# Kernel tuning notes

Hardware: AMD Instinct MI355X
Metric: run time of the kernel (lower is better)

The kernel has to match this reference:

```python
import jax, jax.numpy as jnp
import numpy as np

B, F, E = 1024, 1024, 256      # batch, flat_shape (mobilenet), embedding_size
L1, L2, L3 = 16, 8, 32         # level1 classes, level2 classes per branch, level3 classes per leaf
NE3 = L1 * L2                  # 128 leaf (level-3) classifier heads


def setup_inputs() -> dict:
    key = jax.random.key(0)
    ks = jax.random.split(key, 10)
    w = lambda k, shape: (jax.random.normal(k, shape, jnp.float32) * 0.02)
    return {
        "features_x": jax.random.normal(ks[0], (B, F), jnp.float32),
        "features_y": jax.random.normal(ks[1], (B, F), jnp.float32),
        # level-1 head: Linear(F->E, no bias) + LayerNorm + ReLU + Linear(E->L1)
        "l1_W1": w(ks[2], (F, E)),
        "l1_g": jnp.ones((E,), jnp.float32), "l1_b": jnp.zeros((E,), jnp.float32),
        "l1_W2": w(ks[3], (E, L1)), "l1_b2": jnp.zeros((L1,), jnp.float32),
        # level-2 heads (one per level-1 class), stacked on a leading expert axis
        "l2_W1": w(ks[4], (L1, F, E)),
        "l2_g": jnp.ones((L1, E), jnp.float32), "l2_b": jnp.zeros((L1, E), jnp.float32),
        "l2_W2": w(ks[5], (L1, E, L2)), "l2_b2": jnp.zeros((L1, L2), jnp.float32),
        # level-3 heads (flattened [level1][level2] -> NE3 experts)
        "l3_W1": w(ks[6], (NE3, F, E)),
        "l3_g": jnp.ones((NE3, E), jnp.float32), "l3_b": jnp.zeros((NE3, E), jnp.float32),
        "l3_W2": w(ks[7], (NE3, E, L3)), "l3_b2": jnp.zeros((NE3, L3), jnp.float32),
    }


def _ln(h, g, b, eps=1e-5):
    m = jnp.mean(h, axis=-1, keepdims=True)
    v = jnp.mean(jnp.square(h - m), axis=-1, keepdims=True)
    return (h - m) * jax.lax.rsqrt(v + eps) * g + b


def reference(features_x, features_y,
              l1_W1, l1_g, l1_b, l1_W2, l1_b2,
              l2_W1, l2_g, l2_b, l2_W2, l2_b2,
              l3_W1, l3_g, l3_b, l3_W2, l3_b2):
    # Dropout is identity in eval mode.
    x, y = features_x, features_y
    rows = jnp.arange(x.shape[0])

    # level 1: single head on x
    h1 = jax.nn.relu(_ln(x @ l1_W1, l1_g, l1_b))
    logits1 = h1 @ l1_W2 + l1_b2                                # [B, L1]
    idx1 = jnp.argmax(logits1, axis=-1)                         # argmax(softmax) == argmax

    # level 2: routed head on 0.6*x + 0.4*y; compute all L1 heads batched, gather selected
    ft = 0.6 * x + 0.4 * y
    h2 = jax.nn.relu(_ln(jnp.einsum('bf,efh->beh', ft, l2_W1), l2_g, l2_b))  # [B, L1, E]
    logits2_all = jnp.einsum('beh,ehc->bec', h2, l2_W2) + l2_b2              # [B, L1, L2]
    logits2 = logits2_all[rows, idx1]                                        # [B, L2]
    idx2 = jnp.argmax(logits2, axis=-1)

    # level 3: doubly-routed head on x; flat expert index = idx1*L2 + idx2
    eidx = idx1 * logits2.shape[-1] + idx2
    h3 = jax.nn.relu(_ln(jnp.einsum('bf,efh->beh', x, l3_W1), l3_g, l3_b))   # [B, NE3, E]
    logits3_all = jnp.einsum('beh,ehc->bec', h3, l3_W2) + l3_b2              # [B, NE3, L3]
    logits3 = logits3_all[rows, eidx]                                        # [B, L3]

    # uniform class counts => pad_sequence is a no-op
    return (logits1, logits2, logits3)
```

## Files before the change

### kernel.cpp

```cpp
#include <hip/hip_runtime.h>

#define B_   1024
#define F_   1024
#define E_   256
#define NL1  16
#define NL2  8
#define NL3  32

__device__ __forceinline__ float b2f(unsigned short u) {
    union { unsigned int i; float f; } v;
    v.i = ((unsigned int)u) << 16;
    return v.f;
}

__device__ __forceinline__ unsigned short f2b(float f) {
    union { float f; unsigned int i; } v;
    v.f = f;
    unsigned int x = v.i;
    x += 0x7fffu + ((x >> 16) & 1u);
    return (unsigned short)(x >> 16);
}

template<int NC>
__device__ void head_row(
    const float* __restrict__ in,
    const void* W1, const void* g, const void* b,
    const void* W2, const void* b2v, int bf,
    float* part,
    float* hn,
    float* red,
    float* lg,
    int t)
{
    const int lane = t & 63;
    const int grp  = t >> 6;
    const int e0   = lane * 4;

    float a0 = 0.f, a1 = 0.f, a2 = 0.f, a3 = 0.f;
    if (bf) {
        const unsigned short* W = (const unsigned short*)W1 + (size_t)grp * 256 * E_;
        for (int ii = 0; ii < 256; ii += 16) {
            ushort4 w[16];
            float   xv[16];
            #pragma unroll
            for (int k = 0; k < 16; ++k) {
                w[k]  = *(const ushort4*)(W + (size_t)(ii + k) * E_ + e0);
                xv[k] = in[grp * 256 + ii + k];
            }
            #pragma unroll
            for (int k = 0; k < 16; ++k) {
                a0 += xv[k] * b2f(w[k].x);
                a1 += xv[k] * b2f(w[k].y);
                a2 += xv[k] * b2f(w[k].z);
                a3 += xv[k] * b2f(w[k].w);
            }
        }
    } else {
        const float* W = (const float*)W1 + (size_t)grp * 256 * E_;
        for (int ii = 0; ii < 256; ii += 8) {
            float4 w[8];
            float  xv[8];
            #pragma unroll
            for (int k = 0; k < 8; ++k) {
                w[k]  = *(const float4*)(W + (size_t)(ii + k) * E_ + e0);
                xv[k] = in[grp * 256 + ii + k];
            }
            #pragma unroll
            for (int k = 0; k < 8; ++k) {
                a0 += xv[k] * w[k].x; a1 += xv[k] * w[k].y;
                a2 += xv[k] * w[k].z; a3 += xv[k] * w[k].w;
            }
        }
    }
    part[grp * E_ + e0 + 0] = a0;
    part[grp * E_ + e0 + 1] = a1;
    part[grp * E_ + e0 + 2] = a2;
    part[grp * E_ + e0 + 3] = a3;
    __syncthreads();

    float h = part[0 * E_ + t] + part[1 * E_ + t] + part[2 * E_ + t] + part[3 * E_ + t];

    float s = h, ss = h * h;
    #pragma unroll
    for (int o = 32; o > 0; o >>= 1) {
        s  += __shfl_xor(s, o);
        ss += __shfl_xor(ss, o);
    }
    if (lane == 0) { red[grp * 2 + 0] = s; red[grp * 2 + 1] = ss; }
    __syncthreads();
    float S  = red[0] + red[2] + red[4] + red[6];
    float SS = red[1] + red[3] + red[5] + red[7];
    float m    = S * (1.0f / E_);
    float var  = SS * (1.0f / E_) - m * m;
    float rstd = rsqrtf(var + 1e-5f);

    float gv, bv;
    if (bf) {
        gv = b2f(((const unsigned short*)g)[t]);
        bv = b2f(((const unsigned short*)b)[t]);
    } else {
        gv = ((const float*)g)[t];
        bv = ((const float*)b)[t];
    }
    hn[t] = fmaxf((h - m) * rstd * gv + bv, 0.0f);
    __syncthreads();

    constexpr int G  = 256 / NC;
    constexpr int CH = E_ / G;
    const int c = t % NC;
    const int j = t / NC;
    float a = 0.f;
    if (bf) {
        const unsigned short* W = (const unsigned short*)W2;
        #pragma unroll 8
        for (int e = j * CH; e < j * CH + CH; ++e) a += hn[e] * b2f(W[(size_t)e * NC + c]);
    } else {
        const float* W = (const float*)W2;
        #pragma unroll 8
        for (int e = j * CH; e < j * CH + CH; ++e) a += hn[e] * W[(size_t)e * NC + c];
    }
    part[j * NC + c] = a;
    __syncthreads();
    #pragma unroll
    for (int sr = G / 2; sr > 0; sr >>= 1) {
        if (j < sr) part[j * NC + c] += part[(j + sr) * NC + c];
        __syncthreads();
    }
    if (t < NC) {
        float bias = bf ? b2f(((const unsigned short*)b2v)[t]) : ((const float*)b2v)[t];
        lg[t] = part[t] + bias;
    }
    __syncthreads();
}

__global__ void dtype_sniff_kernel(const unsigned int* l1g_words, int* flag) {
    if (threadIdx.x == 0 && blockIdx.x == 0) {
        *flag = (l1g_words[0] == 0x3F803F80u) ? 1 : 0;
    }
}

__global__ __launch_bounds__(256, 4) void MultiLevelClassifier_26491358282059_kernel(
    const void* x, const void* y,
    const void* l1W1, const void* l1g, const void* l1b,
    const void* l1W2, const void* l1b2,
    const void* l2W1, const void* l2g, const void* l2b,
    const void* l2W2, const void* l2b2,
    const void* l3W1, const void* l3g, const void* l3b,
    const void* l3W2, const void* l3b2,
    void* out, const int* flagp)
{
    __shared__ float xs[F_];
    __shared__ float fs[F_];
    __shared__ float part[4 * E_];
    __shared__ float hn[E_];
    __shared__ float red[8];
    __shared__ float lg[NL3];
    __shared__ int   sel;

    const int t   = threadIdx.x;
    const int row = blockIdx.x;
    const int bf  = *flagp;

    if (bf) {
        ushort4 xv = ((const ushort4*)x)[(size_t)row * 256 + t];
        ushort4 yv = ((const ushort4*)y)[(size_t)row * 256 + t];
        float x0 = b2f(xv.x), x1 = b2f(xv.y), x2 = b2f(xv.z), x3 = b2f(xv.w);
        xs[t * 4 + 0] = x0; xs[t * 4 + 1] = x1; xs[t * 4 + 2] = x2; xs[t * 4 + 3] = x3;
        fs[t * 4 + 0] = 0.6f * x0 + 0.4f * b2f(yv.x);
        fs[t * 4 + 1] = 0.6f * x1 + 0.4f * b2f(yv.y);
        fs[t * 4 + 2] = 0.6f * x2 + 0.4f * b2f(yv.z);
        fs[t * 4 + 3] = 0.6f * x3 + 0.4f * b2f(yv.w);
    } else {
        float4 xv = ((const float4*)x)[(size_t)row * 256 + t];
        float4 yv = ((const float4*)y)[(size_t)row * 256 + t];
        xs[t * 4 + 0] = xv.x; xs[t * 4 + 1] = xv.y; xs[t * 4 + 2] = xv.z; xs[t * 4 + 3] = xv.w;
        fs[t * 4 + 0] = 0.6f * xv.x + 0.4f * yv.x;
        fs[t * 4 + 1] = 0.6f * xv.y + 0.4f * yv.y;
        fs[t * 4 + 2] = 0.6f * xv.z + 0.4f * yv.z;
        fs[t * 4 + 3] = 0.6f * xv.w + 0.4f * yv.w;
    }
    __syncthreads();

    head_row<NL1>(xs, l1W1, l1g, l1b, l1W2, l1b2, bf, part, hn, red, lg, t);
    if (t < NL1) {
        size_t o = (size_t)row * NL1 + t;
        if (bf) ((unsigned short*)out)[o] = f2b(lg[t]);
        else    ((float*)out)[o] = lg[t];
    }
    if (t == 0) {
        float best = lg[0]; int bi = 0;
        for (int c = 1; c < NL1; ++c)
            if (lg[c] > best) { best = lg[c]; bi = c; }
        sel = bi;
    }
    __syncthreads();
    const int i1 = sel;

    {
        const void* W1 = bf ? (const void*)((const unsigned short*)l2W1 + (size_t)i1 * F_ * E_)
                            : (const void*)((const float*)l2W1 + (size_t)i1 * F_ * E_);
        const void* g  = bf ? (const void*)((const unsigned short*)l2g + (size_t)i1 * E_)
                            : (const void*)((const float*)l2g + (size_t)i1 * E_);
        const void* b  = bf ? (const void*)((const unsigned short*)l2b + (size_t)i1 * E_)
                            : (const void*)((const float*)l2b + (size_t)i1 * E_);
        const void* W2 = bf ? (const void*)((const unsigned short*)l2W2 + (size_t)i1 * E_ * NL2)
                            : (const void*)((const float*)l2W2 + (size_t)i1 * E_ * NL2);
        const void* b2 = bf ? (const void*)((const unsigned short*)l2b2 + (size_t)i1 * NL2)
                            : (const void*)((const float*)l2b2 + (size_t)i1 * NL2);
        head_row<NL2>(fs, W1, g, b, W2, b2, bf, part, hn, red, lg, t);
    }
    if (t < NL2) {
        size_t o = (size_t)B_ * NL1 + (size_t)row * NL2 + t;
        if (bf) ((unsigned short*)out)[o] = f2b(lg[t]);
        else    ((float*)out)[o] = lg[t];
    }
    if (t == 0) {
        float best = lg[0]; int bi = 0;
        for (int c = 1; c < NL2; ++c)
            if (lg[c] > best) { best = lg[c]; bi = c; }
        sel = i1 * NL2 + bi;
    }
    __syncthreads();
    const int e3 = sel;

    {
        const void* W1 = bf ? (const void*)((const unsigned short*)l3W1 + (size_t)e3 * F_ * E_)
                            : (const void*)((const float*)l3W1 + (size_t)e3 * F_ * E_);
        const void* g  = bf ? (const void*)((const unsigned short*)l3g + (size_t)e3 * E_)
                            : (const void*)((const float*)l3g + (size_t)e3 * E_);
        const void* b  = bf ? (const void*)((const unsigned short*)l3b + (size_t)e3 * E_)
                            : (const void*)((const float*)l3b + (size_t)e3 * E_);
        const void* W2 = bf ? (const void*)((const unsigned short*)l3W2 + (size_t)e3 * E_ * NL3)
                            : (const void*)((const float*)l3W2 + (size_t)e3 * E_ * NL3);
        const void* b2 = bf ? (const void*)((const unsigned short*)l3b2 + (size_t)e3 * NL3)
                            : (const void*)((const float*)l3b2 + (size_t)e3 * NL3);
        head_row<NL3>(xs, W1, g, b, W2, b2, bf, part, hn, red, lg, t);
    }
    if (t < NL3) {
        size_t o = (size_t)B_ * (NL1 + NL2) + (size_t)row * NL3 + t;
        if (bf) ((unsigned short*)out)[o] = f2b(lg[t]);
        else    ((float*)out)[o] = lg[t];
    }
}

extern "C" void kernel_launch(void* const* d_in, const int* in_sizes, int n_in,
                              void* d_out, int out_size, void* d_ws, size_t ws_size,
                              hipStream_t stream) {
    (void)in_sizes; (void)n_in; (void)out_size; (void)ws_size;

    int* flag = (int*)d_ws;

    dtype_sniff_kernel<<<1, 1, 0, stream>>>((const unsigned int*)d_in[3], flag);

    MultiLevelClassifier_26491358282059_kernel<<<B_, 256, 0, stream>>>(
        d_in[0], d_in[1],
        d_in[2], d_in[3], d_in[4], d_in[5], d_in[6],
        d_in[7], d_in[8], d_in[9], d_in[10], d_in[11],
        d_in[12], d_in[13], d_in[14], d_in[15], d_in[16],
        d_out, flag);
}
```

Measured before the change: 407.1 us.

## Group rows by routed expert into chunks to reuse expert weights across rows

```diff
diff --git a/kernel.cpp b/kernel.cpp
--- a/kernel.cpp
+++ b/kernel.cpp
@@ -1,31 +1,33 @@
 #include <hip/hip_runtime.h>
 
-#define B_   1024
-#define F_   1024
-#define E_   256
-#define NL1  16
-#define NL2  8
-#define NL3  32
+#define B_    1024
+#define F_    1024
+#define E_    256
+#define NL1   16
+#define NL2   8
+#define NL3   32
+#define NE3_  128
+#define CS1   4
+#define CS    8
+#define MAXCH2 160
+#define MAXCH3 256
+#define OUT2_OFF (B_ * NL1)
+#define OUT3_OFF (B_ * (NL1 + NL2))
 
 __device__ __forceinline__ float b2f(unsigned short u) {
-    union { unsigned int i; float f; } v;
-    v.i = ((unsigned int)u) << 16;
-    return v.f;
-}
-
+    union { unsigned int i; float f; } v; v.i = ((unsigned int)u) << 16; return v.f;
+}
 __device__ __forceinline__ unsigned short f2b(float f) {
-    union { float f; unsigned int i; } v;
-    v.f = f;
-    unsigned int x = v.i;
-    x += 0x7fffu + ((x >> 16) & 1u);
+    union { float f; unsigned int i; } v; v.f = f;
+    unsigned int x = v.i; x += 0x7fffu + ((x >> 16) & 1u);
     return (unsigned short)(x >> 16);
 }
 
-template<int NC>
-__device__ void head_row(
+template<int R, int NC>
+__device__ void head_chunk(
     const float* __restrict__ in,
-    const void* W1, const void* g, const void* b,
-    const void* W2, const void* b2v, int bf,
+    const void* W1v, const void* gv_, const void* bv_,
+    const void* W2v, const void* b2v, int bf,
     float* part,
     float* hn,
     float* red,
@@ -36,210 +38,358 @@
     const int grp  = t >> 6;
     const int e0   = lane * 4;
 
-    float a0 = 0.f, a1 = 0.f, a2 = 0.f, a3 = 0.f;
+    float acc[R][4];
+    #pragma unroll
+    for (int r = 0; r < R; ++r) { acc[r][0]=0.f; acc[r][1]=0.f; acc[r][2]=0.f; acc[r][3]=0.f; }
+
+    const float* ing = in + grp * 256;
+
     if (bf) {
-        const unsigned short* W = (const unsigned short*)W1 + (size_t)grp * 256 * E_;
-        for (int ii = 0; ii < 256; ii += 16) {
+        const unsigned short* W = (const unsigned short*)W1v + (size_t)grp * 256 * E_;
+        for (int f0 = 0; f0 < 256; f0 += 16) {
             ushort4 w[16];
-            float   xv[16];
-            #pragma unroll
-            for (int k = 0; k < 16; ++k) {
-                w[k]  = *(const ushort4*)(W + (size_t)(ii + k) * E_ + e0);
-                xv[k] = in[grp * 256 + ii + k];
+            #pragma unroll
+            for (int k = 0; k < 16; ++k)
+                w[k] = *(const ushort4*)(W + (size_t)(f0 + k) * E_ + e0);
+            #pragma unroll
+            for (int q = 0; q < 4; ++q) {
+                float4 xq[R];
+                #pragma unroll
+                for (int r = 0; r < R; ++r)
+                    xq[r] = *(const float4*)(ing + r * F_ + f0 + q * 4);
+                #pragma unroll
+                for (int k2 = 0; k2 < 4; ++k2) {
+                    ushort4 ww = w[q * 4 + k2];
+                    float w0 = b2f(ww.x), w1 = b2f(ww.y), w2 = b2f(ww.z), w3 = b2f(ww.w);
+                    #pragma unroll
+                    for (int r = 0; r < R; ++r) {
+                        float xv = (k2 == 0) ? xq[r].x : (k2 == 1) ? xq[r].y
+                                 : (k2 == 2) ? xq[r].z : xq[r].w;
+                        acc[r][0] += xv * w0; acc[r][1] += xv * w1;
+                        acc[r][2] += xv * w2; acc[r][3] += xv * w3;
+                    }
+                }
             }
-            #pragma unroll
-            for (int k = 0; k < 16; ++k) {
-                a0 += xv[k] * b2f(w[k].x);
-                a1 += xv[k] * b2f(w[k].y);
-                a2 += xv[k] * b2f(w[k].z);
-                a3 += xv[k] * b2f(w[k].w);
+        }
+    } else {
+        const float* W = (const float*)W1v + (size_t)grp * 256 * E_;
+        for (int f0 = 0; f0 < 256; f0 += 8) {
+            float4 w[8];
+            #pragma unroll
+            for (int k = 0; k < 8; ++k)
+                w[k] = *(const float4*)(W + (size_t)(f0 + k) * E_ + e0);
+            #pragma unroll
+            for (int q = 0; q < 2; ++q) {
+                float4 xq[R];
+                #pragma unroll
+                for (int r = 0; r < R; ++r)
+                    xq[r] = *(const float4*)(ing + r * F_ + f0 + q * 4);
+                #pragma unroll
+                for (int k2 = 0; k2 < 4; ++k2) {
+                    float4 ww = w[q * 4 + k2];
+                    #pragma unroll
+                    for (int r = 0; r < R; ++r) {
+                        float xv = (k2 == 0) ? xq[r].x : (k2 == 1) ? xq[r].y
+                                 : (k2 == 2) ? xq[r].z : xq[r].w;
+                        acc[r][0] += xv * ww.x; acc[r][1] += xv * ww.y;
+                        acc[r][2] += xv * ww.z; acc[r][3] += xv * ww.w;
+                    }
+                }
             }
         }
-    } else {
-        const float* W = (const float*)W1 + (size_t)grp * 256 * E_;
-        for (int ii = 0; ii < 256; ii += 8) {
-            float4 w[8];
-            float  xv[8];
-            #pragma unroll
-            for (int k = 0; k < 8; ++k) {
-                w[k]  = *(const float4*)(W + (size_t)(ii + k) * E_ + e0);
-                xv[k] = in[grp * 256 + ii + k];
-            }
-            #pragma unroll
-            for (int k = 0; k < 8; ++k) {
-                a0 += xv[k] * w[k].x; a1 += xv[k] * w[k].y;
-                a2 += xv[k] * w[k].z; a3 += xv[k] * w[k].w;
-            }
-        }
-    }
-    part[grp * E_ + e0 + 0] = a0;
-    part[grp * E_ + e0 + 1] = a1;
-    part[grp * E_ + e0 + 2] = a2;
-    part[grp * E_ + e0 + 3] = a3;
-    __syncthreads();
-
-    float h = part[0 * E_ + t] + part[1 * E_ + t] + part[2 * E_ + t] + part[3 * E_ + t];
-
-    float s = h, ss = h * h;
-    #pragma unroll
-    for (int o = 32; o > 0; o >>= 1) {
-        s  += __shfl_xor(s, o);
-        ss += __shfl_xor(ss, o);
-    }
-    if (lane == 0) { red[grp * 2 + 0] = s; red[grp * 2 + 1] = ss; }
-    __syncthreads();
-    float S  = red[0] + red[2] + red[4] + red[6];
-    float SS = red[1] + red[3] + red[5] + red[7];
-    float m    = S * (1.0f / E_);
-    float var  = SS * (1.0f / E_) - m * m;
-    float rstd = rsqrtf(var + 1e-5f);
+    }
+
+    #pragma unroll
+    for (int r = 0; r < R; ++r) {
+        part[(size_t)(grp * R + r) * E_ + e0 + 0] = acc[r][0];
+        part[(size_t)(grp * R + r) * E_ + e0 + 1] = acc[r][1];
+        part[(size_t)(grp * R + r) * E_ + e0 + 2] = acc[r][2];
+        part[(size_t)(grp * R + r) * E_ + e0 + 3] = acc[r][3];
+    }
+    __syncthreads();
+
+    float h[R];
+    #pragma unroll
+    for (int r = 0; r < R; ++r)
+        h[r] = part[(0 * R + r) * E_ + t] + part[(1 * R + r) * E_ + t]
+             + part[(2 * R + r) * E_ + t] + part[(3 * R + r) * E_ + t];
+
+    #pragma unroll
+    for (int r = 0; r < R; ++r) {
+        float s = h[r], ss = h[r] * h[r];
+        #pragma unroll
+        for (int o = 32; o > 0; o >>= 1) { s += __shfl_xor(s, o); ss += __shfl_xor(ss, o); }
+        if (lane == 0) { red[(grp * R + r) * 2 + 0] = s; red[(grp * R + r) * 2 + 1] = ss; }
+    }
+    __syncthreads();
 
     float gv, bv;
-    if (bf) {
-        gv = b2f(((const unsigned short*)g)[t]);
-        bv = b2f(((const unsigned short*)b)[t]);
-    } else {
-        gv = ((const float*)g)[t];
-        bv = ((const float*)b)[t];
-    }
-    hn[t] = fmaxf((h - m) * rstd * gv + bv, 0.0f);
-    __syncthreads();
-
-    constexpr int G  = 256 / NC;
+    if (bf) { gv = b2f(((const unsigned short*)gv_)[t]); bv = b2f(((const unsigned short*)bv_)[t]); }
+    else    { gv = ((const float*)gv_)[t];               bv = ((const float*)bv_)[t]; }
+
+    #pragma unroll
+    for (int r = 0; r < R; ++r) {
+        float S  = red[(0*R+r)*2] + red[(1*R+r)*2] + red[(2*R+r)*2] + red[(3*R+r)*2];
+        float SS = red[(0*R+r)*2+1] + red[(1*R+r)*2+1] + red[(2*R+r)*2+1] + red[(3*R+r)*2+1];
+        float m    = S * (1.0f / E_);
+        float var  = SS * (1.0f / E_) - m * m;
+        float rstd = rsqrtf(var + 1e-5f);
+        hn[r * E_ + t] = fmaxf((h[r] - m) * rstd * gv + bv, 0.0f);
+    }
+    __syncthreads();
+
+    constexpr int RN = R * NC;
+    constexpr int G  = 256 / RN;
     constexpr int CH = E_ / G;
-    const int c = t % NC;
-    const int j = t / NC;
+    const int oi = t % RN, j = t / RN, r = oi / NC, c = oi % NC;
     float a = 0.f;
     if (bf) {
-        const unsigned short* W = (const unsigned short*)W2;
+        const unsigned short* W = (const unsigned short*)W2v;
         #pragma unroll 8
-        for (int e = j * CH; e < j * CH + CH; ++e) a += hn[e] * b2f(W[(size_t)e * NC + c]);
+        for (int e = j * CH; e < j * CH + CH; ++e) a += hn[r * E_ + e] * b2f(W[(size_t)e * NC + c]);
     } else {
-        const float* W = (const float*)W2;
+        const float* W = (const float*)W2v;
         #pragma unroll 8
-        for (int e = j * CH; e < j * CH + CH; ++e) a += hn[e] * W[(size_t)e * NC + c];
-    }
-    part[j * NC + c] = a;
-    __syncthreads();
-    #pragma unroll
-    for (int sr = G / 2; sr > 0; sr >>= 1) {
-        if (j < sr) part[j * NC + c] += part[(j + sr) * NC + c];
+        for (int e = j * CH; e < j * CH + CH; ++e) a += hn[r * E_ + e] * W[(size_t)e * NC + c];
+    }
+    float bias = bf ? b2f(((const unsigned short*)b2v)[c]) : ((const float*)b2v)[c];
+    if (G > 1) {
+        part[t] = a;
         __syncthreads();
-    }
-    if (t < NC) {
-        float bias = bf ? b2f(((const unsigned short*)b2v)[t]) : ((const float*)b2v)[t];
-        lg[t] = part[t] + bias;
+        if (j == 0) {
+            float sum = a;
+            #pragma unroll
+            for (int jj = 1; jj < G; ++jj) sum += part[jj * RN + oi];
+            lg[oi] = sum + bias;
+        }
+    } else {
+        lg[oi] = a + bias;
     }
     __syncthreads();
 }
 
 __global__ void dtype_sniff_kernel(const unsigned int* l1g_words, int* flag) {
-    if (threadIdx.x == 0 && blockIdx.x == 0) {
+    if (threadIdx.x == 0 && blockIdx.x == 0)
         *flag = (l1g_words[0] == 0x3F803F80u) ? 1 : 0;
-    }
-}
-
-__global__ __launch_bounds__(256, 4) void MultiLevelClassifier_26491358282059_kernel(
+}
+
+__global__ __launch_bounds__(256) void mlc_level1_kernel(
+    const void* x, const void* W1, const void* g, const void* b,
+    const void* W2, const void* b2, void* out, int* idx1, const int* flagp)
+{
+    __shared__ float in_s[CS1 * F_];
+    __shared__ float part[4 * CS1 * E_];
+    __shared__ float hn[CS1 * E_];
+    __shared__ float red[4 * CS1 * 2];
+    __shared__ float lg[CS1 * NL1];
+
+    const int t = threadIdx.x;
+    const int bf = *flagp;
+    const int row0 = blockIdx.x * CS1;
+
+    #pragma unroll
+    for (int r = 0; r < CS1; ++r) {
+        if (bf) {
+            ushort4 xv = ((const ushort4*)x)[(size_t)(row0 + r) * 256 + t];
+            in_s[r * F_ + t*4+0] = b2f(xv.x); in_s[r * F_ + t*4+1] = b2f(xv.y);
+            in_s[r * F_ + t*4+2] = b2f(xv.z); in_s[r * F_ + t*4+3] = b2f(xv.w);
+        } else {
+            float4 xv = ((const float4*)x)[(size_t)(row0 + r) * 256 + t];
+            in_s[r * F_ + t*4+0] = xv.x; in_s[r * F_ + t*4+1] = xv.y;
+            in_s[r * F_ + t*4+2] = xv.z; in_s[r * F_ + t*4+3] = xv.w;
+        }
+    }
+    __syncthreads();
+
+    head_chunk<CS1, NL1>(in_s, W1, g, b, W2, b2, bf, part, hn, red, lg, t);
+
+    if (t < CS1 * NL1) {
+        int r = t / NL1, c = t % NL1;
+        size_t o = (size_t)(row0 + r) * NL1 + c;
+        if (bf) ((unsigned short*)out)[o] = f2b(lg[t]);
+        else    ((float*)out)[o] = lg[t];
+        if (c == 0) {
+            float best = lg[r * NL1]; int bi = 0;
+            #pragma unroll
+            for (int cc = 1; cc < NL1; ++cc)
+                if (lg[r * NL1 + cc] > best) { best = lg[r * NL1 + cc]; bi = cc; }
+            idx1[row0 + r] = bi;
+        }
+    }
+}
+
+template<int NEXP, int MAXCH>
+__global__ __launch_bounds__(1024) void mlc_route_kernel(
+    const int* __restrict__ src, int* __restrict__ rows_out, int4* __restrict__ chunks_out)
+{
+    __shared__ int hist[NEXP], offs[NEXP], cur[NEXP];
+    const int t = threadIdx.x;
+    if (t < NEXP) hist[t] = 0;
+    __syncthreads();
+    int e = src[t];
+    if (e < 0) e = 0; if (e >= NEXP) e = NEXP - 1;
+    atomicAdd(&hist[e], 1);
+    __syncthreads();
+    if (t == 0) {
+        int o = 0;
+        for (int i = 0; i < NEXP; ++i) { offs[i] = o; cur[i] = o; o += hist[i]; }
+    }
+    __syncthreads();
+    int pos = atomicAdd(&cur[e], 1);
+    if (pos >= 0 && pos < B_) rows_out[pos] = t;
+    if (t == 0) {
+        int nch = 0;
+        for (int i = 0; i < NEXP; ++i) {
+            int n = hist[i], st = offs[i];
+            for (int j = 0; j < n && nch < MAXCH; j += CS)
+                chunks_out[nch++] = make_int4(i, st + j, min(CS, n - j), 0);
+        }
+        for (; nch < MAXCH; ++nch) chunks_out[nch] = make_int4(0, 0, 0, 0);
+    }
+}
+
+__global__ __launch_bounds__(256) void mlc_level2_kernel(
     const void* x, const void* y,
-    const void* l1W1, const void* l1g, const void* l1b,
-    const void* l1W2, const void* l1b2,
-    const void* l2W1, const void* l2g, const void* l2b,
-    const void* l2W2, const void* l2b2,
-    const void* l3W1, const void* l3g, const void* l3b,
-    const void* l3W2, const void* l3b2,
+    const void* W1b, const void* gb, const void* bb,
+    const void* W2b, const void* b2b,
+    const int4* __restrict__ chunks, const int* __restrict__ rowlist,
+    void* out, int* eidx, const int* flagp)
+{
+    __shared__ float in_s[CS * F_];
+    __shared__ float part[4 * CS * E_];
+    __shared__ float hn[CS * E_];
+    __shared__ float red[4 * CS * 2];
+    __shared__ float lg[CS * NL2];
+    __shared__ int4  chs;
+    __shared__ int   rows_s[CS];
+
+    const int t = threadIdx.x;
+    const int bf = *flagp;
+
+    if (t == 0) chs = chunks[blockIdx.x];
+    __syncthreads();
+    const int expert = chs.x, start = chs.y, count = chs.z;
+    if (count <= 0) return;
+    if (t < CS) rows_s[t] = (t < count) ? rowlist[start + t] : -1;
+    __syncthreads();
+
+    #pragma unroll
+    for (int r = 0; r < CS; ++r) {
+        int row = rows_s[r];
+        float f0 = 0.f, f1 = 0.f, f2 = 0.f, f3 = 0.f;
+        if (row >= 0) {
+            if (bf) {
+                ushort4 xv = ((const ushort4*)x)[(size_t)row * 256 + t];
+                ushort4 yv = ((const ushort4*)y)[(size_t)row * 256 + t];
+                f0 = 0.6f * b2f(xv.x) + 0.4f * b2f(yv.x);
+                f1 = 0.6f * b2f(xv.y) + 0.4f * b2f(yv.y);
+                f2 = 0.6f * b2f(xv.z) + 0.4f * b2f(yv.z);
+                f3 = 0.6f * b2f(xv.w) + 0.4f * b2f(yv.w);
+            } else {
+                float4 xv = ((const float4*)x)[(size_t)row * 256 + t];
+                float4 yv = ((const float4*)y)[(size_t)row * 256 + t];
+                f0 = 0.6f * xv.x + 0.4f * yv.x; f1 = 0.6f * xv.y + 0.4f * yv.y;
+                f2 = 0.6f * xv.z + 0.4f * yv.z; f3 = 0.6f * xv.w + 0.4f * yv.w;
+            }
+        }
+        in_s[r * F_ + t*4+0] = f0; in_s[r * F_ + t*4+1] = f1;
+        in_s[r * F_ + t*4+2] = f2; in_s[r * F_ + t*4+3] = f3;
+    }
+    __syncthreads();
+
+    const void* W1 = bf ? (const void*)((const unsigned short*)W1b + (size_t)expert * F_ * E_)
+                        : (const void*)((const float*)W1b + (size_t)expert * F_ * E_);
+    const void* g  = bf ? (const void*)((const unsigned short*)gb + (size_t)expert * E_)
+                        : (const void*)((const float*)gb + (size_t)expert * E_);
+    const void* b  = bf ? (const void*)((const unsigned short*)bb + (size_t)expert * E_)
+                        : (const void*)((const float*)bb + (size_t)expert * E_);
+    const void* W2 = bf ? (const void*)((const unsigned short*)W2b + (size_t)expert * E_ * NL2)
+                        : (const void*)((const float*)W2b + (size_t)expert * E_ * NL2);
+    const void* b2 = bf ? (const void*)((const unsigned short*)b2b + (size_t)expert * NL2)
+                        : (const void*)((const float*)b2b + (size_t)expert * NL2);
+
+    head_chunk<CS, NL2>(in_s, W1, g, b, W2, b2, bf, part, hn, red, lg, t);
+
+    if (t < CS * NL2) {
+        int r = t / NL2, c = t % NL2;
+        if (r < count) {
+            size_t o = (size_t)OUT2_OFF + (size_t)rows_s[r] * NL2 + c;
+            if (bf) ((unsigned short*)out)[o] = f2b(lg[t]);
+            else    ((float*)out)[o] = lg[t];
+            if (c == 0) {
+                float best = lg[r * NL2]; int bi = 0;
+                #pragma unroll
+                for (int cc = 1; cc < NL2; ++cc)
+                    if (lg[r * NL2 + cc] > best) { best = lg[r * NL2 + cc]; bi = cc; }
+                eidx[rows_s[r]] = expert * NL2 + bi;
+            }
+        }
+    }
+}
+
+__global__ __launch_bounds__(256) void MultiLevelClassifier_26491358282059_kernel(
+    const void* x,
+    const void* W1b, const void* gb, const void* bb,
+    const void* W2b, const void* b2b,
+    const int4* __restrict__ chunks, const int* __restrict__ rowlist,
     void* out, const int* flagp)
 {
-    __shared__ float xs[F_];
-    __shared__ float fs[F_];
-    __shared__ float part[4 * E_];
-    __shared__ float hn[E_];
-    __shared__ float red[8];
-    __shared__ float lg[NL3];
-    __shared__ int   sel;
-
-    const int t   = threadIdx.x;
-    const int row = blockIdx.x;
-    const int bf  = *flagp;
-
-    if (bf) {
-        ushort4 xv = ((const ushort4*)x)[(size_t)row * 256 + t];
-        ushort4 yv = ((const ushort4*)y)[(size_t)row * 256 + t];
-        float x0 = b2f(xv.x), x1 = b2f(xv.y), x2 = b2f(xv.z), x3 = b2f(xv.w);
-        xs[t * 4 + 0] = x0; xs[t * 4 + 1] = x1; xs[t * 4 + 2] = x2; xs[t * 4 + 3] = x3;
-        fs[t * 4 + 0] = 0.6f * x0 + 0.4f * b2f(yv.x);
-        fs[t * 4 + 1] = 0.6f * x1 + 0.4f * b2f(yv.y);
-        fs[t * 4 + 2] = 0.6f * x2 + 0.4f * b2f(yv.z);
-        fs[t * 4 + 3] = 0.6f * x3 + 0.4f * b2f(yv.w);
-    } else {
-        float4 xv = ((const float4*)x)[(size_t)row * 256 + t];
-        float4 yv = ((const float4*)y)[(size_t)row * 256 + t];
-        xs[t * 4 + 0] = xv.x; xs[t * 4 + 1] = xv.y; xs[t * 4 + 2] = xv.z; xs[t * 4 + 3] = xv.w;
-        fs[t * 4 + 0] = 0.6f * xv.x + 0.4f * yv.x;
-        fs[t * 4 + 1] = 0.6f * xv.y + 0.4f * yv.y;
-        fs[t * 4 + 2] = 0.6f * xv.z + 0.4f * yv.z;
-        fs[t * 4 + 3] = 0.6f * xv.w + 0.4f * yv.w;
-    }
-    __syncthreads();
-
-    head_row<NL1>(xs, l1W1, l1g, l1b, l1W2, l1b2, bf, part, hn, red, lg, t);
-    if (t < NL1) {
-        size_t o = (size_t)row * NL1 + t;
-        if (bf) ((unsigned short*)out)[o] = f2b(lg[t]);
-        else    ((float*)out)[o] = lg[t];
-    }
-    if (t == 0) {
-        float best = lg[0]; int bi = 0;
-        for (int c = 1; c < NL1; ++c)
-            if (lg[c] > best) { best = lg[c]; bi = c; }
-        sel = bi;
-    }
-    __syncthreads();
-    const int i1 = sel;
-
-    {
-        const void* W1 = bf ? (const void*)((const unsigned short*)l2W1 + (size_t)i1 * F_ * E_)
-                            : (const void*)((const float*)l2W1 + (size_t)i1 * F_ * E_);
-        const void* g  = bf ? (const void*)((const unsigned short*)l2g + (size_t)i1 * E_)
-                            : (const void*)((const float*)l2g + (size_t)i1 * E_);
-        const void* b  = bf ? (const void*)((const unsigned short*)l2b + (size_t)i1 * E_)
-                            : (const void*)((const float*)l2b + (size_t)i1 * E_);
-        const void* W2 = bf ? (const void*)((const unsigned short*)l2W2 + (size_t)i1 * E_ * NL2)
-                            : (const void*)((const float*)l2W2 + (size_t)i1 * E_ * NL2);
-        const void* b2 = bf ? (const void*)((const unsigned short*)l2b2 + (size_t)i1 * NL2)
-                            : (const void*)((const float*)l2b2 + (size_t)i1 * NL2);
-        head_row<NL2>(fs, W1, g, b, W2, b2, bf, part, hn, red, lg, t);
-    }
-    if (t < NL2) {
-        size_t o = (size_t)B_ * NL1 + (size_t)row * NL2 + t;
-        if (bf) ((unsigned short*)out)[o] = f2b(lg[t]);
-        else    ((float*)out)[o] = lg[t];
-    }
-    if (t == 0) {
-        float best = lg[0]; int bi = 0;
-        for (int c = 1; c < NL2; ++c)
-            if (lg[c] > best) { best = lg[c]; bi = c; }
-        sel = i1 * NL2 + bi;
-    }
-    __syncthreads();
-    const int e3 = sel;
-
-    {
-        const void* W1 = bf ? (const void*)((const unsigned short*)l3W1 + (size_t)e3 * F_ * E_)
-                            : (const void*)((const float*)l3W1 + (size_t)e3 * F_ * E_);
-        const void* g  = bf ? (const void*)((const unsigned short*)l3g + (size_t)e3 * E_)
-                            : (const void*)((const float*)l3g + (size_t)e3 * E_);
-        const void* b  = bf ? (const void*)((const unsigned short*)l3b + (size_t)e3 * E_)
-                            : (const void*)((const float*)l3b + (size_t)e3 * E_);
-        const void* W2 = bf ? (const void*)((const unsigned short*)l3W2 + (size_t)e3 * E_ * NL3)
-                            : (const void*)((const float*)l3W2 + (size_t)e3 * E_ * NL3);
-        const void* b2 = bf ? (const void*)((const unsigned short*)l3b2 + (size_t)e3 * NL3)
-                            : (const void*)((const float*)l3b2 + (size_t)e3 * NL3);
-        head_row<NL3>(xs, W1, g, b, W2, b2, bf, part, hn, red, lg, t);
-    }
-    if (t < NL3) {
-        size_t o = (size_t)B_ * (NL1 + NL2) + (size_t)row * NL3 + t;
-        if (bf) ((unsigned short*)out)[o] = f2b(lg[t]);
-        else    ((float*)out)[o] = lg[t];
+    __shared__ float in_s[CS * F_];
+    __shared__ float part[4 * CS * E_];
+    __shared__ float hn[CS * E_];
+    __shared__ float red[4 * CS * 2];
+    __shared__ float lg[CS * NL3];
+    __shared__ int4  chs;
+    __shared__ int   rows_s[CS];
+
+    const int t = threadIdx.x;
+    const int bf = *flagp;
+
+    if (t == 0) chs = chunks[blockIdx.x];
+    __syncthreads();
+    const int expert = chs.x, start = chs.y, count = chs.z;
+    if (count <= 0) return;
+    if (t < CS) rows_s[t] = (t < count) ? rowlist[start + t] : -1;
+    __syncthreads();
+
+    #pragma unroll
+    for (int r = 0; r < CS; ++r) {
+        int row = rows_s[r];
+        float f0 = 0.f, f1 = 0.f, f2 = 0.f, f3 = 0.f;
+        if (row >= 0) {
+            if (bf) {
+                ushort4 xv = ((const ushort4*)x)[(size_t)row * 256 + t];
+                f0 = b2f(xv.x); f1 = b2f(xv.y); f2 = b2f(xv.z); f3 = b2f(xv.w);
+            } else {
+                float4 xv = ((const float4*)x)[(size_t)row * 256 + t];
+                f0 = xv.x; f1 = xv.y; f2 = xv.z; f3 = xv.w;
+            }
+        }
+        in_s[r * F_ + t*4+0] = f0; in_s[r * F_ + t*4+1] = f1;
+        in_s[r * F_ + t*4+2] = f2; in_s[r * F_ + t*4+3] = f3;
+    }
+    __syncthreads();
+
+    const void* W1 = bf ? (const void*)((const unsigned short*)W1b + (size_t)expert * F_ * E_)
+                        : (const void*)((const float*)W1b + (size_t)expert * F_ * E_);
+    const void* g  = bf ? (const void*)((const unsigned short*)gb + (size_t)expert * E_)
+                        : (const void*)((const float*)gb + (size_t)expert * E_);
+    const void* b  = bf ? (const void*)((const unsigned short*)bb + (size_t)expert * E_)
+                        : (const void*)((const float*)bb + (size_t)expert * E_);
+    const void* W2 = bf ? (const void*)((const unsigned short*)W2b + (size_t)expert * E_ * NL3)
+                        : (const void*)((const float*)W2b + (size_t)expert * E_ * NL3);
+    const void* b2 = bf ? (const void*)((const unsigned short*)b2b + (size_t)expert * NL3)
+                        : (const void*)((const float*)b2b + (size_t)expert * NL3);
+
+    head_chunk<CS, NL3>(in_s, W1, g, b, W2, b2, bf, part, hn, red, lg, t);
+
+    if (t < CS * NL3) {
+        int r = t / NL3, c = t % NL3;
+        if (r < count) {
+            size_t o = (size_t)OUT3_OFF + (size_t)rows_s[r] * NL3 + c;
+            if (bf) ((unsigned short*)out)[o] = f2b(lg[t]);
+            else    ((float*)out)[o] = lg[t];
+        }
     }
 }
 
@@ -248,14 +398,30 @@
                               hipStream_t stream) {
     (void)in_sizes; (void)n_in; (void)out_size; (void)ws_size;
 
-    int* flag = (int*)d_ws;
+    int* ws = (int*)d_ws;
+    int*  flag  = ws;
+    int*  idx1  = ws + 64;
+    int*  eidx  = ws + 1088;
+    int*  rows2 = ws + 2112;
+    int*  rows3 = ws + 3136;
+    int4* ch2   = (int4*)(ws + 4160);
+    int4* ch3   = (int4*)(ws + 4160 + MAXCH2 * 4);
 
     dtype_sniff_kernel<<<1, 1, 0, stream>>>((const unsigned int*)d_in[3], flag);
 
-    MultiLevelClassifier_26491358282059_kernel<<<B_, 256, 0, stream>>>(
-        d_in[0], d_in[1],
-        d_in[2], d_in[3], d_in[4], d_in[5], d_in[6],
-        d_in[7], d_in[8], d_in[9], d_in[10], d_in[11],
-        d_in[12], d_in[13], d_in[14], d_in[15], d_in[16],
-        d_out, flag);
-}
+    mlc_level1_kernel<<<B_ / CS1, 256, 0, stream>>>(
+        d_in[0], d_in[2], d_in[3], d_in[4], d_in[5], d_in[6],
+        d_out, idx1, flag);
+
+    mlc_route_kernel<NL1, MAXCH2><<<1, 1024, 0, stream>>>(idx1, rows2, ch2);
+
+    mlc_level2_kernel<<<MAXCH2, 256, 0, stream>>>(
+        d_in[0], d_in[1], d_in[7], d_in[8], d_in[9], d_in[10], d_in[11],
+        ch2, rows2, d_out, eidx, flag);
+
+    mlc_route_kernel<NE3_, MAXCH3><<<1, 1024, 0, stream>>>(eidx, rows3, ch3);
+
+    MultiLevelClassifier_26491358282059_kernel<<<MAXCH3, 256, 0, stream>>>(
+        d_in[0], d_in[12], d_in[13], d_in[14], d_in[15], d_in[16],
+        ch3, rows3, d_out, flag);
+}
```

After: 344.6 us. 1.18x faster.
